# Kernel optimization log

Measured on AMD Instinct MI355X. Metric: run time of the kernel, lower is better.

Reference implementation:

```python
import jax, jax.numpy as jnp
import numpy as np

S = 256
H = 4       # n_heads
DH = 32     # head_dim
D = H * DH  # model dim
EPS = 1e-5


def setup_inputs() -> dict:
    key = jax.random.key(0)
    ks = jax.random.split(key, 12)
    x = jax.random.normal(ks[0], (1, S, S, D), dtype=jnp.float32)
    # attention mask: mostly 0, occasionally large negative (masked)
    keep = jax.random.uniform(ks[1], (1, 1, S, S)) < 0.9
    attn_mask = jnp.where(keep, 0.0, -1e9).astype(jnp.float32)
    sc = 1.0 / np.sqrt(D)
    ln_w = jnp.ones((D,), jnp.float32)
    ln_b = jnp.zeros((D,), jnp.float32)
    Wb = jax.random.normal(ks[2], (H, D), jnp.float32) * sc   # bias projection (linear.weight)
    Wq = jax.random.normal(ks[3], (D, D), jnp.float32) * sc
    Wk = jax.random.normal(ks[4], (D, D), jnp.float32) * sc
    Wv = jax.random.normal(ks[5], (D, D), jnp.float32) * sc
    Wg = jax.random.normal(ks[6], (D, D), jnp.float32) * sc
    Wo = jax.random.normal(ks[7], (D, D), jnp.float32) * sc
    return {"x": x, "attn_mask": attn_mask, "ln_w": ln_w, "ln_b": ln_b,
            "Wb": Wb, "Wq": Wq, "Wk": Wk, "Wv": Wv, "Wg": Wg, "Wo": Wo}


def reference(x, attn_mask, ln_w, ln_b, Wb, Wq, Wk, Wv, Wg, Wo):
    # x: [1,S,S,D] pair representation; ending=False so no transpose of S axes.
    x0 = x[0]  # [S,S,D]
    mu = jnp.mean(x0, axis=-1, keepdims=True)
    var = jnp.mean(jnp.square(x0 - mu), axis=-1, keepdims=True)
    xn = (x0 - mu) * jax.lax.rsqrt(var + EPS) * ln_w + ln_b  # [S,S,D]

    # triangle bias: [S,S,H] -> [1,H,S,S] (broadcast over batch-of-rows)
    bias = jnp.einsum('bqd,hd->hbq', xn, Wb)[None]  # [1,H,S,S]

    def heads(W):
        return jnp.einsum('bqd,ed->bqe', xn, W).reshape(S, S, H, DH).transpose(0, 2, 1, 3)

    q, k, v = heads(Wq), heads(Wk), heads(Wv)  # each [S,H,S,DH]

    scale = 1.0 / np.sqrt(DH)
    scores = jnp.einsum('bhqd,bhkd->bhqk', q, k) * scale + bias + attn_mask  # [S,H,S,S]
    attn = jax.nn.softmax(scores, axis=-1)
    o = jnp.einsum('bhqk,bhkd->bhqd', attn, v)  # [S,H,S,DH]
    o = o.transpose(0, 2, 1, 3).reshape(S, S, D)

    g = jnp.einsum('bqd,ed->bqe', xn, Wg)
    out = jnp.einsum('bqe,fe->bqf', o * jax.nn.sigmoid(g), Wo)  # [S,S,D]
    return out[None]  # [1,S,S,D]
```

## Files before the change

kernel.cpp:

```cpp
#include <hip/hip_runtime.h>
#include <hip/hip_bf16.h>

#define S_DIM 256
#define D_DIM 128
#define H_DIM 4
#define NPOS  (S_DIM * S_DIM)

typedef __attribute__((ext_vector_type(8))) short  short8;
typedef __attribute__((ext_vector_type(4))) float  f32x4;

__device__ __forceinline__ float b2f(unsigned short u) {
    union { float f; unsigned int u32; } c; c.u32 = ((unsigned int)u) << 16; return c.f;
}
__device__ __forceinline__ unsigned short f2b(float f) {
    __hip_bfloat16 h = __float2bfloat16(f);
    return *reinterpret_cast<unsigned short*>(&h);
}

__global__ __launch_bounds__(256) void ln_biasmask_kernel(
    const float* __restrict__ x, const float* __restrict__ mask,
    const float* __restrict__ lnw, const float* __restrict__ lnb,
    const float* __restrict__ Wb, float* __restrict__ bm)
{
    const int wave = threadIdx.x >> 6, lane = threadIdx.x & 63;
    const int p = blockIdx.x * 4 + wave;

    float2 v = ((const float2*)x)[p * 64 + lane];
    float s = v.x + v.y, ss = v.x * v.x + v.y * v.y;
    #pragma unroll
    for (int m = 1; m < 64; m <<= 1) { s += __shfl_xor(s, m); ss += __shfl_xor(ss, m); }
    float mean = s * (1.f / 128.f);
    float var  = ss * (1.f / 128.f) - mean * mean;
    float rstd = rsqrtf(var + 1e-5f);

    float xn0 = (v.x - mean) * rstd * lnw[lane * 2]     + lnb[lane * 2];
    float xn1 = (v.y - mean) * rstd * lnw[lane * 2 + 1] + lnb[lane * 2 + 1];

    float mval = mask[p];
    #pragma unroll
    for (int h = 0; h < H_DIM; h++) {
        float d = xn0 * Wb[h * 128 + lane * 2] + xn1 * Wb[h * 128 + lane * 2 + 1];
        #pragma unroll
        for (int m = 1; m < 64; m <<= 1) d += __shfl_xor(d, m);
        if (lane == 0) bm[(long)h * NPOS + p] = d + mval;
    }
}

__global__ __launch_bounds__(256) void proj_ln_kernel(
    const float* __restrict__ x,
    const float* __restrict__ lnw, const float* __restrict__ lnb,
    const float* __restrict__ Wq, const float* __restrict__ Wk,
    const float* __restrict__ Wv, const float* __restrict__ Wg,
    int p0, unsigned short* __restrict__ strip)
{
    __shared__ __align__(16) unsigned short A_lds[64 * 136];
    __shared__ __align__(16) unsigned short W_lds[128 * 136];
    const int tid = threadIdx.x;
    const int m0 = blockIdx.x * 64;
    const int gy = blockIdx.y;
    const float* W = (gy == 0) ? Wq : (gy == 1) ? Wk : (gy == 2) ? Wv : Wg;

    const int lr = tid >> 4, c8 = (tid & 15) * 8;
    #pragma unroll
    for (int i = 0; i < 4; i++) {
        int row = lr + i * 16;
        const float* src = x + (size_t)(p0 + m0 + row) * 128 + c8;
        float4 f0 = *(const float4*)(src);
        float4 f1 = *(const float4*)(src + 4);
        float s  = f0.x + f0.y + f0.z + f0.w + f1.x + f1.y + f1.z + f1.w;
        float ss = f0.x*f0.x + f0.y*f0.y + f0.z*f0.z + f0.w*f0.w
                 + f1.x*f1.x + f1.y*f1.y + f1.z*f1.z + f1.w*f1.w;
        #pragma unroll
        for (int m = 1; m < 16; m <<= 1) { s += __shfl_xor(s, m); ss += __shfl_xor(ss, m); }
        float mean = s * (1.f / 128.f);
        float var  = ss * (1.f / 128.f) - mean * mean;
        float rstd = rsqrtf(var + 1e-5f);
        float xv[8] = {f0.x, f0.y, f0.z, f0.w, f1.x, f1.y, f1.z, f1.w};
        unsigned short pk[8];
        #pragma unroll
        for (int j = 0; j < 8; j++)
            pk[j] = f2b((xv[j] - mean) * rstd * lnw[c8 + j] + lnb[c8 + j]);
        *(uint4*)(&A_lds[row * 136 + c8]) = *(const uint4*)pk;
    }
    #pragma unroll
    for (int i = 0; i < 8; i++) {
        int wr = lr + i * 16;
        const float* src = W + (size_t)wr * 128 + c8;
        float4 f0 = *(const float4*)(src);
        float4 f1 = *(const float4*)(src + 4);
        unsigned short pk[8] = {f2b(f0.x), f2b(f0.y), f2b(f0.z), f2b(f0.w),
                                f2b(f1.x), f2b(f1.y), f2b(f1.z), f2b(f1.w)};
        *(uint4*)(&W_lds[wr * 136 + c8]) = *(const uint4*)pk;
    }
    __syncthreads();

    const int w = tid >> 6, lane = tid & 63;
    const int l16 = lane & 15, quad = lane >> 4;
    f32x4 acc[8];
    #pragma unroll
    for (int nt = 0; nt < 8; nt++) acc[nt] = (f32x4){0.f, 0.f, 0.f, 0.f};

    #pragma unroll
    for (int k0 = 0; k0 < 128; k0 += 32) {
        short8 a = *(const short8*)(&A_lds[(w * 16 + l16) * 136 + k0 + quad * 8]);
        #pragma unroll
        for (int nt = 0; nt < 8; nt++) {
            short8 b = *(const short8*)(&W_lds[(nt * 16 + l16) * 136 + k0 + quad * 8]);
            acc[nt] = __builtin_amdgcn_mfma_f32_16x16x32_bf16(b, a, acc[nt], 0, 0, 0);
        }
    }

    const size_t rowbase = (size_t)(m0 + w * 16 + l16) * 512 + gy * 128;
    #pragma unroll
    for (int nt = 0; nt < 8; nt++) {
        uint2 pk;
        pk.x = (unsigned)f2b(acc[nt][0]) | ((unsigned)f2b(acc[nt][1]) << 16);
        pk.y = (unsigned)f2b(acc[nt][2]) | ((unsigned)f2b(acc[nt][3]) << 16);
        *(uint2*)(&strip[rowbase + nt * 16 + quad * 4]) = pk;
    }
}

__global__ __launch_bounds__(256) void attn_kernel(
    const unsigned short* __restrict__ strip, const float* __restrict__ bm,
    int b0, unsigned short* __restrict__ gated)
{
    __shared__ __align__(16) unsigned short VT_lds[32 * 264];
    __shared__ __align__(16) unsigned short P_lds[4 * 16 * 264];
    const int bl = blockIdx.x, h = blockIdx.y, z = blockIdx.z;
    const int b  = b0 + bl;
    const int tid = threadIdx.x;

    {
        const int row = tid >> 2, chunk = (tid & 3) * 8;
        #pragma unroll
        for (int i = 0; i < 4; i++) {
            int rr = row + i * 64;
            uint4 v = *(const uint4*)(strip + (size_t)(bl * 256 + rr) * 512 + 256 + h * 32 + chunk);
            unsigned short vs[8] = {
                (unsigned short)(v.x & 0xffff), (unsigned short)(v.x >> 16),
                (unsigned short)(v.y & 0xffff), (unsigned short)(v.y >> 16),
                (unsigned short)(v.z & 0xffff), (unsigned short)(v.z >> 16),
                (unsigned short)(v.w & 0xffff), (unsigned short)(v.w >> 16)};
            #pragma unroll
            for (int j = 0; j < 8; j++) VT_lds[(chunk + j) * 264 + rr] = vs[j];
        }
    }
    __syncthreads();

    const int w = tid >> 6, lane = tid & 63;
    const int l16 = lane & 15, quad = lane >> 4;
    const float* bmh = bm + (long)h * NPOS;
    unsigned short* P_w = P_lds + w * 16 * 264;
    const float scale = 0.17677669529663687f;

    #pragma unroll 1
    for (int i = 0; i < 2; i++) {
        const int q0 = (w * 4 + z * 2 + i) * 16;
        short8 bq = *(const short8*)(strip + (size_t)(bl * 256 + q0 + l16) * 512 + h * 32 + quad * 8);
        const float* brow = bmh + (size_t)(q0 + l16) * 256 + quad * 4;

        float sc[16][4];
        #pragma unroll
        for (int nt = 0; nt < 16; nt++) {
            short8 ka = *(const short8*)(strip + (size_t)(bl * 256 + nt * 16 + l16) * 512 + 128 + h * 32 + quad * 8);
            f32x4 c = (f32x4){0.f, 0.f, 0.f, 0.f};
            c = __builtin_amdgcn_mfma_f32_16x16x32_bf16(ka, bq, c, 0, 0, 0);
            float4 bb = *(const float4*)(brow + nt * 16);
            sc[nt][0] = c[0] * scale + bb.x;
            sc[nt][1] = c[1] * scale + bb.y;
            sc[nt][2] = c[2] * scale + bb.z;
            sc[nt][3] = c[3] * scale + bb.w;
        }

        float m0 = sc[0][0], m1 = sc[0][1], m2 = sc[0][2], m3 = sc[0][3];
        #pragma unroll
        for (int nt = 1; nt < 16; nt++) {
            m0 = fmaxf(m0, sc[nt][0]); m1 = fmaxf(m1, sc[nt][1]);
            m2 = fmaxf(m2, sc[nt][2]); m3 = fmaxf(m3, sc[nt][3]);
        }
        float m = fmaxf(fmaxf(m0, m1), fmaxf(m2, m3));
        m = fmaxf(m, __shfl_xor(m, 16));
        m = fmaxf(m, __shfl_xor(m, 32));

        float s0 = 0.f, s1 = 0.f, s2 = 0.f, s3 = 0.f;
        #pragma unroll
        for (int nt = 0; nt < 16; nt++) {
            float p0_ = __expf(sc[nt][0] - m); sc[nt][0] = p0_; s0 += p0_;
            float p1_ = __expf(sc[nt][1] - m); sc[nt][1] = p1_; s1 += p1_;
            float p2_ = __expf(sc[nt][2] - m); sc[nt][2] = p2_; s2 += p2_;
            float p3_ = __expf(sc[nt][3] - m); sc[nt][3] = p3_; s3 += p3_;
        }
        float ssum = (s0 + s1) + (s2 + s3);
        ssum += __shfl_xor(ssum, 16);
        ssum += __shfl_xor(ssum, 32);
        float inv = 1.f / ssum;

        #pragma unroll
        for (int nt = 0; nt < 16; nt++) {
            uint2 pk;
            pk.x = (unsigned)f2b(sc[nt][0]) | ((unsigned)f2b(sc[nt][1]) << 16);
            pk.y = (unsigned)f2b(sc[nt][2]) | ((unsigned)f2b(sc[nt][3]) << 16);
            *(uint2*)(&P_w[l16 * 264 + nt * 16 + quad * 4]) = pk;
        }

        f32x4 oacc[2];
        oacc[0] = (f32x4){0.f, 0.f, 0.f, 0.f};
        oacc[1] = (f32x4){0.f, 0.f, 0.f, 0.f};
        #pragma unroll
        for (int kt = 0; kt < 8; kt++) {
            short8 pa = *(const short8*)(&P_w[l16 * 264 + kt * 32 + quad * 8]);
            #pragma unroll
            for (int nh = 0; nh < 2; nh++) {
                short8 vb = *(const short8*)(&VT_lds[(nh * 16 + l16) * 264 + kt * 32 + quad * 8]);
                oacc[nh] = __builtin_amdgcn_mfma_f32_16x16x32_bf16(pa, vb, oacc[nh], 0, 0, 0);
            }
        }
        #pragma unroll
        for (int rr = 0; rr < 4; rr++) {
            float invr = __shfl(inv, quad * 4 + rr);
            int row = q0 + quad * 4 + rr;
            #pragma unroll
            for (int nh = 0; nh < 2; nh++) {
                int cl = nh * 16 + l16;
                float g = b2f(strip[(size_t)(bl * 256 + row) * 512 + 384 + h * 32 + cl]);
                float ov = oacc[nh][rr] * invr;
                ov = ov / (1.f + __expf(-g));
                gated[((size_t)b * 256 + row) * 128 + h * 32 + cl] = f2b(ov);
            }
        }
    }
}

__global__ __launch_bounds__(256) void outproj_mfma_kernel(
    const unsigned short* __restrict__ gated, const float* __restrict__ Wo,
    float* __restrict__ out)
{
    __shared__ __align__(16) unsigned short A_lds[64 * 136];
    __shared__ __align__(16) unsigned short W_lds[128 * 136];
    const int tid = threadIdx.x;
    const int m0 = blockIdx.x * 64;

    const int lr = tid >> 4, c8 = (tid & 15) * 8;
    #pragma unroll
    for (int i = 0; i < 4; i++) {
        int row = lr + i * 16;
        *(uint4*)(&A_lds[row * 136 + c8]) =
            *(const uint4*)(gated + (size_t)(m0 + row) * 128 + c8);
    }
    #pragma unroll
    for (int i = 0; i < 8; i++) {
        const float* src = Wo + (size_t)(lr + i * 16) * 128 + c8;
        float4 f0 = *(const float4*)(src);
        float4 f1 = *(const float4*)(src + 4);
        unsigned short pk[8] = {f2b(f0.x), f2b(f0.y), f2b(f0.z), f2b(f0.w),
                                f2b(f1.x), f2b(f1.y), f2b(f1.z), f2b(f1.w)};
        *(uint4*)(&W_lds[(lr + i * 16) * 136 + c8]) = *(const uint4*)pk;
    }
    __syncthreads();

    const int w = tid >> 6, lane = tid & 63;
    const int l16 = lane & 15, quad = lane >> 4;
    f32x4 acc[8];
    #pragma unroll
    for (int nt = 0; nt < 8; nt++) acc[nt] = (f32x4){0.f, 0.f, 0.f, 0.f};

    #pragma unroll
    for (int k0 = 0; k0 < 128; k0 += 32) {
        short8 a = *(const short8*)(&A_lds[(w * 16 + l16) * 136 + k0 + quad * 8]);
        #pragma unroll
        for (int nt = 0; nt < 8; nt++) {
            short8 b = *(const short8*)(&W_lds[(nt * 16 + l16) * 136 + k0 + quad * 8]);
            acc[nt] = __builtin_amdgcn_mfma_f32_16x16x32_bf16(b, a, acc[nt], 0, 0, 0);
        }
    }

    float* orow = out + (size_t)(m0 + w * 16 + l16) * 128;
    #pragma unroll
    for (int nt = 0; nt < 8; nt++)
        *(f32x4*)(&orow[nt * 16 + quad * 4]) = acc[nt];
}

extern "C" void kernel_launch(void* const* d_in, const int* in_sizes, int n_in,
                              void* d_out, int out_size, void* d_ws, size_t ws_size,
                              hipStream_t stream)
{
    (void)in_sizes; (void)n_in; (void)out_size;
    const float* x    = (const float*)d_in[0];
    const float* mask = (const float*)d_in[1];
    const float* lnw  = (const float*)d_in[2];
    const float* lnb  = (const float*)d_in[3];
    const float* Wb   = (const float*)d_in[4];
    const float* Wq   = (const float*)d_in[5];
    const float* Wk   = (const float*)d_in[6];
    const float* Wv   = (const float*)d_in[7];
    const float* Wg   = (const float*)d_in[8];
    const float* Wo   = (const float*)d_in[9];
    float* out = (float*)d_out;

    const size_t bmB = (size_t)H_DIM * NPOS * sizeof(float);
    const size_t gB  = (size_t)NPOS * 128 * sizeof(unsigned short);
    int HB = 256;
    while (HB > 16 && bmB + gB + (size_t)HB * 256 * 512 * 2 > ws_size) HB >>= 1;

    char* ws = (char*)d_ws;
    float*          bm    = (float*)ws;
    unsigned short* gated = (unsigned short*)(ws + bmB);
    unsigned short* strip = (unsigned short*)(ws + bmB + gB);

    ln_biasmask_kernel<<<NPOS / 4, 256, 0, stream>>>(x, mask, lnw, lnb, Wb, bm);
    for (int b0 = 0; b0 < S_DIM; b0 += HB) {
        proj_ln_kernel<<<dim3(HB * 4, 4), 256, 0, stream>>>(
            x, lnw, lnb, Wq, Wk, Wv, Wg, b0 * 256, strip);
        attn_kernel<<<dim3(HB, H_DIM, 2), 256, 0, stream>>>(strip, bm, b0, gated);
    }
    outproj_mfma_kernel<<<NPOS / 64, 256, 0, stream>>>(gated, Wo, out);
}
```

Baseline: 245.4 us.

## Write V transposed from projection kernel and drop LDS transpose in attention

The projection kernel now computes V with swapped MFMA operands and writes it directly in transposed [b, h*32+d, k] layout to a separate buffer, while Q/K/G are packed into a narrower 384-wide strip. The attention kernel reads V^T straight from global memory instead of staging and transposing it through LDS, and each block now handles all 16 query tiles (grid z dimension removed). This removes the scattered LDS transpose and the block-wide sync but halves the number of attention blocks and relies on cache hits for repeated V global loads.

New measurement: 241.7 us. About the same (-1.5%).

```diff
diff --git a/kernel.cpp b/kernel.cpp
--- a/kernel.cpp
+++ b/kernel.cpp
@@ -5,6 +5,7 @@
 #define D_DIM 128
 #define H_DIM 4
 #define NPOS  (S_DIM * S_DIM)
+#define SW    384
 
 typedef __attribute__((ext_vector_type(8))) short  short8;
 typedef __attribute__((ext_vector_type(4))) float  f32x4;
@@ -51,7 +52,7 @@
     const float* __restrict__ lnw, const float* __restrict__ lnb,
     const float* __restrict__ Wq, const float* __restrict__ Wk,
     const float* __restrict__ Wv, const float* __restrict__ Wg,
-    int p0, unsigned short* __restrict__ strip)
+    int p0, unsigned short* __restrict__ strip, unsigned short* __restrict__ vt)
 {
     __shared__ __align__(16) unsigned short A_lds[64 * 136];
     __shared__ __align__(16) unsigned short W_lds[128 * 136];
@@ -100,69 +101,72 @@
     #pragma unroll
     for (int nt = 0; nt < 8; nt++) acc[nt] = (f32x4){0.f, 0.f, 0.f, 0.f};
 
-    #pragma unroll
-    for (int k0 = 0; k0 < 128; k0 += 32) {
-        short8 a = *(const short8*)(&A_lds[(w * 16 + l16) * 136 + k0 + quad * 8]);
+    if (gy == 2) {
+        #pragma unroll
+        for (int k0 = 0; k0 < 128; k0 += 32) {
+            short8 a = *(const short8*)(&A_lds[(w * 16 + l16) * 136 + k0 + quad * 8]);
+            #pragma unroll
+            for (int nt = 0; nt < 8; nt++) {
+                short8 b = *(const short8*)(&W_lds[(nt * 16 + l16) * 136 + k0 + quad * 8]);
+                acc[nt] = __builtin_amdgcn_mfma_f32_16x16x32_bf16(a, b, acc[nt], 0, 0, 0);
+            }
+        }
+        const int blv = m0 >> 8;
+        const int kl  = (m0 & 255) + w * 16 + quad * 4;
         #pragma unroll
         for (int nt = 0; nt < 8; nt++) {
-            short8 b = *(const short8*)(&W_lds[(nt * 16 + l16) * 136 + k0 + quad * 8]);
-            acc[nt] = __builtin_amdgcn_mfma_f32_16x16x32_bf16(b, a, acc[nt], 0, 0, 0);
-        }
-    }
-
-    const size_t rowbase = (size_t)(m0 + w * 16 + l16) * 512 + gy * 128;
-    #pragma unroll
-    for (int nt = 0; nt < 8; nt++) {
-        uint2 pk;
-        pk.x = (unsigned)f2b(acc[nt][0]) | ((unsigned)f2b(acc[nt][1]) << 16);
-        pk.y = (unsigned)f2b(acc[nt][2]) | ((unsigned)f2b(acc[nt][3]) << 16);
-        *(uint2*)(&strip[rowbase + nt * 16 + quad * 4]) = pk;
+            uint2 pk;
+            pk.x = (unsigned)f2b(acc[nt][0]) | ((unsigned)f2b(acc[nt][1]) << 16);
+            pk.y = (unsigned)f2b(acc[nt][2]) | ((unsigned)f2b(acc[nt][3]) << 16);
+            *(uint2*)(&vt[((size_t)(blv * 128 + nt * 16 + l16)) * 256 + kl]) = pk;
+        }
+    } else {
+        #pragma unroll
+        for (int k0 = 0; k0 < 128; k0 += 32) {
+            short8 a = *(const short8*)(&A_lds[(w * 16 + l16) * 136 + k0 + quad * 8]);
+            #pragma unroll
+            for (int nt = 0; nt < 8; nt++) {
+                short8 b = *(const short8*)(&W_lds[(nt * 16 + l16) * 136 + k0 + quad * 8]);
+                acc[nt] = __builtin_amdgcn_mfma_f32_16x16x32_bf16(b, a, acc[nt], 0, 0, 0);
+            }
+        }
+        const int off = (gy == 0) ? 0 : (gy == 1) ? 128 : 256;
+        const size_t rowbase = (size_t)(m0 + w * 16 + l16) * SW + off;
+        #pragma unroll
+        for (int nt = 0; nt < 8; nt++) {
+            uint2 pk;
+            pk.x = (unsigned)f2b(acc[nt][0]) | ((unsigned)f2b(acc[nt][1]) << 16);
+            pk.y = (unsigned)f2b(acc[nt][2]) | ((unsigned)f2b(acc[nt][3]) << 16);
+            *(uint2*)(&strip[rowbase + nt * 16 + quad * 4]) = pk;
+        }
     }
 }
 
 __global__ __launch_bounds__(256) void attn_kernel(
-    const unsigned short* __restrict__ strip, const float* __restrict__ bm,
-    int b0, unsigned short* __restrict__ gated)
-{
-    __shared__ __align__(16) unsigned short VT_lds[32 * 264];
+    const unsigned short* __restrict__ strip, const unsigned short* __restrict__ vt,
+    const float* __restrict__ bm, int b0, unsigned short* __restrict__ gated)
+{
     __shared__ __align__(16) unsigned short P_lds[4 * 16 * 264];
-    const int bl = blockIdx.x, h = blockIdx.y, z = blockIdx.z;
+    const int bl = blockIdx.x, h = blockIdx.y;
     const int b  = b0 + bl;
     const int tid = threadIdx.x;
-
-    {
-        const int row = tid >> 2, chunk = (tid & 3) * 8;
-        #pragma unroll
-        for (int i = 0; i < 4; i++) {
-            int rr = row + i * 64;
-            uint4 v = *(const uint4*)(strip + (size_t)(bl * 256 + rr) * 512 + 256 + h * 32 + chunk);
-            unsigned short vs[8] = {
-                (unsigned short)(v.x & 0xffff), (unsigned short)(v.x >> 16),
-                (unsigned short)(v.y & 0xffff), (unsigned short)(v.y >> 16),
-                (unsigned short)(v.z & 0xffff), (unsigned short)(v.z >> 16),
-                (unsigned short)(v.w & 0xffff), (unsigned short)(v.w >> 16)};
-            #pragma unroll
-            for (int j = 0; j < 8; j++) VT_lds[(chunk + j) * 264 + rr] = vs[j];
-        }
-    }
-    __syncthreads();
-
     const int w = tid >> 6, lane = tid & 63;
     const int l16 = lane & 15, quad = lane >> 4;
     const float* bmh = bm + (long)h * NPOS;
+    const unsigned short* vth = vt + ((size_t)bl * 128 + h * 32) * 256;
     unsigned short* P_w = P_lds + w * 16 * 264;
     const float scale = 0.17677669529663687f;
 
     #pragma unroll 1
-    for (int i = 0; i < 2; i++) {
-        const int q0 = (w * 4 + z * 2 + i) * 16;
-        short8 bq = *(const short8*)(strip + (size_t)(bl * 256 + q0 + l16) * 512 + h * 32 + quad * 8);
+    for (int i = 0; i < 4; i++) {
+        const int q0 = (w * 4 + i) * 16;
+        short8 bq = *(const short8*)(strip + (size_t)(bl * 256 + q0 + l16) * SW + h * 32 + quad * 8);
         const float* brow = bmh + (size_t)(q0 + l16) * 256 + quad * 4;
 
         float sc[16][4];
         #pragma unroll
         for (int nt = 0; nt < 16; nt++) {
-            short8 ka = *(const short8*)(strip + (size_t)(bl * 256 + nt * 16 + l16) * 512 + 128 + h * 32 + quad * 8);
+            short8 ka = *(const short8*)(strip + (size_t)(bl * 256 + nt * 16 + l16) * SW + 128 + h * 32 + quad * 8);
             f32x4 c = (f32x4){0.f, 0.f, 0.f, 0.f};
             c = __builtin_amdgcn_mfma_f32_16x16x32_bf16(ka, bq, c, 0, 0, 0);
             float4 bb = *(const float4*)(brow + nt * 16);
@@ -211,7 +215,7 @@
             short8 pa = *(const short8*)(&P_w[l16 * 264 + kt * 32 + quad * 8]);
             #pragma unroll
             for (int nh = 0; nh < 2; nh++) {
-                short8 vb = *(const short8*)(&VT_lds[(nh * 16 + l16) * 264 + kt * 32 + quad * 8]);
+                short8 vb = *(const short8*)(vth + (size_t)(nh * 16 + l16) * 256 + kt * 32 + quad * 8);
                 oacc[nh] = __builtin_amdgcn_mfma_f32_16x16x32_bf16(pa, vb, oacc[nh], 0, 0, 0);
             }
         }
@@ -222,7 +226,7 @@
             #pragma unroll
             for (int nh = 0; nh < 2; nh++) {
                 int cl = nh * 16 + l16;
-                float g = b2f(strip[(size_t)(bl * 256 + row) * 512 + 384 + h * 32 + cl]);
+                float g = b2f(strip[(size_t)(bl * 256 + row) * SW + 256 + h * 32 + cl]);
                 float ov = oacc[nh][rr] * invr;
                 ov = ov / (1.f + __expf(-g));
                 gated[((size_t)b * 256 + row) * 128 + h * 32 + cl] = f2b(ov);
@@ -297,21 +301,23 @@
     const float* Wo   = (const float*)d_in[9];
     float* out = (float*)d_out;
 
-    const size_t bmB = (size_t)H_DIM * NPOS * sizeof(float);
-    const size_t gB  = (size_t)NPOS * 128 * sizeof(unsigned short);
+    const size_t bmB   = (size_t)H_DIM * NPOS * sizeof(float);
+    const size_t gB    = (size_t)NPOS * 128 * sizeof(unsigned short);
+    const size_t perRow = (size_t)256 * SW * 2 + (size_t)128 * 256 * 2;
     int HB = 256;
-    while (HB > 16 && bmB + gB + (size_t)HB * 256 * 512 * 2 > ws_size) HB >>= 1;
+    while (HB > 16 && bmB + gB + (size_t)HB * perRow > ws_size) HB >>= 1;
 
     char* ws = (char*)d_ws;
     float*          bm    = (float*)ws;
     unsigned short* gated = (unsigned short*)(ws + bmB);
-    unsigned short* strip = (unsigned short*)(ws + bmB + gB);
+    unsigned short* vt    = (unsigned short*)(ws + bmB + gB);
+    unsigned short* strip = vt + (size_t)HB * 128 * 256;
 
     ln_biasmask_kernel<<<NPOS / 4, 256, 0, stream>>>(x, mask, lnw, lnb, Wb, bm);
     for (int b0 = 0; b0 < S_DIM; b0 += HB) {
         proj_ln_kernel<<<dim3(HB * 4, 4), 256, 0, stream>>>(
-            x, lnw, lnb, Wq, Wk, Wv, Wg, b0 * 256, strip);
-        attn_kernel<<<dim3(HB, H_DIM, 2), 256, 0, stream>>>(strip, bm, b0, gated);
+            x, lnw, lnb, Wq, Wk, Wv, Wg, b0 * 256, strip, vt);
+        attn_kernel<<<dim3(HB, H_DIM), 256, 0, stream>>>(strip, vt, bm, b0, gated);
     }
     outproj_mfma_kernel<<<NPOS / 64, 256, 0, stream>>>(gated, Wo, out);
 }
```
